# Kernel tuning notes

Hardware: AMD Instinct MI355X
Metric: run time of the kernel (lower is better)

Reference implementation:

```python
import jax, jax.numpy as jnp
import numpy as np

SQRT2 = 1.4142135623730951
T, B, C, H, W = 4, 8, 256, 32, 32
NB, D = 16, 16  # FL_blocks, block_size = dim // FL_blocks
VTH = 0.5       # all l1/l2 spike thresholds default to 0.5
TAUS = (0.01, 0.02, 0.02, 0.05)  # l2 channel-sparsity taus for LL,HL,LH,HH

# Heaviside spike with ATan surrogate gradient (spikingjelly default, alpha=2)
@jax.custom_vjp
def spike(x):
    return (x >= 0.0).astype(x.dtype)

def _spike_fwd(x):
    return spike(x), x

def _spike_bwd(x, g):
    alpha = 2.0
    sg = (alpha / 2.0) / (1.0 + (jnp.pi / 2.0 * alpha * x) ** 2)
    return (g * sg,)

spike.defvjp(_spike_fwd, _spike_bwd)

def lif(x, tau=2.0):
    # MultiStepLIFNode: v += (x - v)/tau, fire at vth=1, hard reset, detach_reset
    def step(v, xt):
        v = v + (xt - v) / tau
        s = spike(v - 1.0)
        v = v * (1.0 - jax.lax.stop_gradient(s))
        return v, s
    _, s = jax.lax.scan(step, jnp.zeros_like(x[0]), x)
    return s

def bn(x, g, b, eps=1e-5):
    # BatchNorm2d in training mode (batch statistics), x: (N,C,H,W)
    m = x.mean((0, 2, 3), keepdims=True)
    v = x.var((0, 2, 3), keepdims=True)
    return (x - m) / jnp.sqrt(v + eps) * g[None, :, None, None] + b[None, :, None, None]

def conv2d(x, w, b):
    y = jax.lax.conv_general_dilated(x, w, (1, 1), 'SAME',
                                     dimension_numbers=('NCHW', 'OIHW', 'NCHW'))
    return y + b[None, :, None, None]

def coeff_gate(c, vth):
    # spike-thresholded wavelet coefficient: keep coeff where |coeff| >= vth
    return c * spike(jnp.abs(c) - vth)

def channel_gate(c, tau):
    # 'channel' sparsity mode: drop whole channels whose mean energy < tau
    e = jnp.mean(c * c, axis=(0, 1, 3, 4))
    return c * spike(e - tau)[None, None, :, None, None]

def fwd(x, haar_weight, conv1_w, conv1_b, conv2_w, conv2_b,
        g_fwd, b_fwd, g_mul, b_mul, g_inv, b_inv, g_c1, b_c1, g_c2, b_c2):
    Tn, Bn, Cn, Hn, Wn = x.shape
    H2, W2 = Hn // 2, Wn // 2
    TB = Tn * Bn
    xs = lif(x)
    # level-1 Haar along W, spike-gated low/high subbands -> (T,B,2C,H,W/2)
    lo = (xs[..., 0::2] + xs[..., 1::2]) / SQRT2
    hi = (xs[..., 0::2] - xs[..., 1::2]) / SQRT2
    h1 = jnp.concatenate([coeff_gate(lo, VTH), coeff_gate(hi, VTH)], axis=2)
    h1 = bn(h1.reshape(TB, 2 * Cn, Hn, W2), g_fwd, b_fwd).reshape(Tn, Bn, 2 * Cn, Hn, W2)
    # level-2 Haar along H -> LL,HL,LH,HH each (T,B,C,H/2,W/2)
    L, Hc = h1[:, :, :Cn], h1[:, :, Cn:]
    def hh(t):
        return ((t[:, :, :, 0::2] + t[:, :, :, 1::2]) / SQRT2,
                (t[:, :, :, 0::2] - t[:, :, :, 1::2]) / SQRT2)
    LL, HL = hh(L)
    LH, HH = hh(Hc)
    subs = [channel_gate(coeff_gate(c, VTH), tau)
            for c, tau in zip((LL, HL, LH, HH), TAUS)]
    h2 = jnp.concatenate(subs, axis=2)  # (T,B,4C,H/2,W/2)
    h2 = bn(h2.reshape(TB, 4 * Cn, H2, W2), g_mul, b_mul).reshape(Tn, Bn, 4 * Cn, H2, W2)
    # block-diagonal mixing: exactly the torch reshape/permute/einsum path
    haar = h2.reshape(TB, NB, 4 * D, H2, W2).transpose(0, 3, 4, 1, 2)  # (TB,H2,W2,NB,4D)
    parts = [jnp.einsum('thwbd,bdk->thwbk', haar[..., i * D:(i + 1) * D], haar_weight)
             for i in range(4)]
    haar = jnp.concatenate(parts, axis=-1)
    haar = haar.reshape(TB, H2, W2, 4 * Cn).transpose(0, 3, 1, 2).reshape(Tn, Bn, 4 * Cn, H2, W2)
    # inverse 2-level Haar -> (T,B,C,H,W)
    LLr, HLr, LHr, HHr = (haar[:, :, i * Cn:(i + 1) * Cn] for i in range(4))
    def inv_h(a, b):
        e = (a + b) / SQRT2
        o = (a - b) / SQRT2
        return jnp.stack([e, o], axis=-2).reshape(Tn, Bn, Cn, Hn, W2)
    Lr = inv_h(LLr, HLr)
    Hr = inv_h(LHr, HHr)
    e = (Lr + Hr) / SQRT2
    o = (Lr - Hr) / SQRT2
    rec = jnp.stack([e, o], axis=-1).reshape(Tn, Bn, Cn, Hn, Wn)
    rec = bn(rec.reshape(TB, Cn, Hn, Wn), g_inv, b_inv).reshape(Tn, Bn, Cn, Hn, Wn)
    # per-block conv residual branches on the spike tensor
    xr = xs.reshape(TB * NB, D, Hn, Wn)
    c1 = bn(conv2d(xr, conv1_w, conv1_b).reshape(TB, Cn, Hn, Wn), g_c1, b_c1).reshape(Tn, Bn, Cn, Hn, Wn)
    c2 = bn(conv2d(xr, conv2_w, conv2_b).reshape(TB, Cn, Hn, Wn), g_c2, b_c2).reshape(Tn, Bn, Cn, Hn, Wn)
    return rec + c1 + c2

def setup_inputs() -> dict:
    key = jax.random.key(0)
    ks = jax.random.split(key, 4)
    return {
        'x': jax.random.normal(ks[0], (T, B, C, H, W), jnp.float32),
        'haar_weight': 0.02 * jax.random.normal(ks[1], (NB, D, D), jnp.float32),
        'conv1_w': 0.1 * jax.random.normal(ks[2], (D, D, 1, 1), jnp.float32),
        'conv1_b': jnp.zeros((D,), jnp.float32),
        'conv2_w': 0.05 * jax.random.normal(ks[3], (D, D, 3, 3), jnp.float32),
        'conv2_b': jnp.zeros((D,), jnp.float32),
        'g_fwd': jnp.ones((2 * C,), jnp.float32), 'b_fwd': jnp.zeros((2 * C,), jnp.float32),
        'g_mul': jnp.ones((4 * C,), jnp.float32), 'b_mul': jnp.zeros((4 * C,), jnp.float32),
        'g_inv': jnp.ones((C,), jnp.float32), 'b_inv': jnp.zeros((C,), jnp.float32),
        'g_c1': jnp.ones((C,), jnp.float32), 'b_c1': jnp.zeros((C,), jnp.float32),
        'g_c2': jnp.ones((C,), jnp.float32), 'b_c2': jnp.zeros((C,), jnp.float32),
    }

def reference(x, haar_weight, conv1_w, conv1_b, conv2_w, conv2_b,
              g_fwd, b_fwd, g_mul, b_mul, g_inv, b_inv, g_c1, b_c1, g_c2, b_c2):
    return fwd(x, haar_weight, conv1_w, conv1_b, conv2_w, conv2_b,
               g_fwd, b_fwd, g_mul, b_mul, g_inv, b_inv, g_c1, b_c1, g_c2, b_c2)
```

## Files before the change

kernel.cpp:

```cpp
#include <hip/hip_runtime.h>

#define T_ 4
#define B_ 8
#define C_ 256
#define TB_ 32
#define SQRT2_ 1.4142135623730951
#define INVS2_ 0.7071067811865475
#define EPS_ 1e-5

typedef __attribute__((ext_vector_type(8))) short short8;
typedef __attribute__((ext_vector_type(4))) float f32x4;

#define XST_OFF  ((size_t)0)
#define H1C_OFF  ((size_t)16777216)
#define COEF_OFF ((size_t)25165824)
#define ST_OFF   ((size_t)41943040)
#define WTAB_OFF ((size_t)42532864)
#define HIST_OFF ((size_t)42555392)
#define S3S 3072
#define S3Q 3328
#define S4S 3584
#define S4Q 3840
#define S5S 4096
#define S5Q 4352
#define NST 4608
#define NREP 16

__device__ __forceinline__ unsigned short f2bf(float v) {
    union { float f; unsigned u; } x; x.f = v;
    unsigned r = x.u + 0x7FFFu + ((x.u >> 16) & 1u);
    return (unsigned short)(r >> 16);
}

__device__ __forceinline__ double st_sum(const double* __restrict__ st, int idx) {
    double s = 0.0;
    #pragma unroll
    for (int r = 0; r < NREP; ++r) s += st[r * NST + idx];
    return s;
}

__device__ __forceinline__ unsigned long long shflx64(unsigned long long v, int m) {
    const unsigned lo_ = __shfl_xor((unsigned)v, m, 64);
    const unsigned hi_ = __shfl_xor((unsigned)(v >> 32), m, 64);
    return ((unsigned long long)hi_ << 32) | lo_;
}

__device__ __forceinline__ void mix_frags_q(const float* __restrict__ hw, int gbq, int lane, short8 am[4]) {
    const int o = lane & 15, g = lane >> 4;
    #pragma unroll
    for (int q = 0; q < 4; ++q) {
        #pragma unroll
        for (int e = 0; e < 8; ++e) {
            const int kk = g * 8 + e;
            unsigned short v = 0;
            if ((kk >> 4) == (q & 1)) {
                const int d = kk & 15;
                const int nbp = q * 4 + gbq;
                v = f2bf(hw[(nbp * 16 + d) * 16 + o]);
            }
            am[q][e] = (short)v;
        }
    }
}

__device__ __forceinline__ void conv_frags(const float* __restrict__ w1, const float* __restrict__ w2w,
                                           int lane, short8* awc2, short8& awc1) {
    const int o = lane & 15, g = lane >> 4, dA = (g & 1) * 8;
    #pragma unroll
    for (int m = 0; m < 5; ++m) {
        const int t = (m < 4) ? (2 * m + (g >> 1)) : 8;
        const bool act = (m < 4) || (g < 2);
        #pragma unroll
        for (int j = 0; j < 8; ++j) {
            const float wv = act ? w2w[(o * 16 + dA + j) * 9 + t] : 0.0f;
            awc2[m][j] = (short)f2bf(wv);
        }
    }
    #pragma unroll
    for (int j = 0; j < 8; ++j) {
        const float wv = (g < 2) ? w1[o * 16 + dA + j] : 0.0f;
        awc1[j] = (short)f2bf(wv);
    }
}

__global__ __launch_bounds__(256) void kwprep(const float* __restrict__ w1, const float* __restrict__ w2w,
                                              const float* __restrict__ hw,
                                              unsigned short* __restrict__ convW,
                                              unsigned short* __restrict__ mixW,
                                              double* __restrict__ st,
                                              int* __restrict__ hist) {
    const int tid = threadIdx.x;
    if (blockIdx.x < 72) {
        const size_t i = ((size_t)blockIdx.x * 256 + tid) * 4;
        double2 z2; z2.x = 0.0; z2.y = 0.0;
        *(double2*)(st + i) = z2;
        *(double2*)(st + i + 2) = z2;
        if (blockIdx.x == 0) {
            const int lane = tid & 63, grp = tid >> 6;
            if (grp == 0) {
                short8 awc2[5], awc1;
                conv_frags(w1, w2w, lane, awc2, awc1);
                #pragma unroll
                for (int m = 0; m < 5; ++m) *(short8*)&convW[(m * 64 + lane) * 8] = awc2[m];
                *(short8*)&convW[(5 * 64 + lane) * 8] = awc1;
            }
            short8 am[4];
            mix_frags_q(hw, grp, lane, am);
            #pragma unroll
            for (int q = 0; q < 4; ++q) *(short8*)&mixW[((grp * 4 + q) * 64 + lane) * 8] = am[q];
        }
    } else {
        const int bi = blockIdx.x - 72;
        uint4* h4 = (uint4*)hist;
        const uint4 z = make_uint4(0u, 0u, 0u, 0u);
        h4[bi * 512 + tid * 2] = z;
        h4[bi * 512 + tid * 2 + 1] = z;
    }
}

__device__ __forceinline__ void load_conv_frags(const unsigned short* __restrict__ convW,
                                                int lane, short8* awc2, short8& awc1) {
    #pragma unroll
    for (int m = 0; m < 5; ++m) awc2[m] = *(const short8*)&convW[(m * 64 + lane) * 8];
    awc1 = *(const short8*)&convW[(5 * 64 + lane) * 8];
}
__device__ __forceinline__ void load_mix_frags(const unsigned short* __restrict__ mixW,
                                               int gbq, int lane, short8 am[4]) {
    #pragma unroll
    for (int q = 0; q < 4; ++q) am[q] = *(const short8*)&mixW[((gbq * 4 + q) * 64 + lane) * 8];
}

__global__ __launch_bounds__(256) void k1_lif(const float* __restrict__ x,
                                              unsigned short* __restrict__ xsT,
                                              signed char* __restrict__ h1c,
                                              int* __restrict__ hist) {
    const int q = blockIdx.x & 3, nb = (blockIdx.x >> 2) & 15, b = blockIdx.x >> 6;
    const int tid = threadIdx.x;
    const int d = tid >> 4, pg = tid & 15;
    const int c = nb * 16 + d;
    const int h = q * 8 + (pg >> 1), wseg = (pg & 1) * 16;
    __shared__ __align__(16) char tr[8192];
    double v[16];
    #pragma unroll
    for (int i = 0; i < 16; ++i) v[i] = 0.0;
    unsigned long long cs = 0, cdd = 0, cu = 0, cv = 0;
    for (int t = 0; t < T_; ++t) {
        const size_t xi = ((size_t)((t * 8 + b) * 256 + c)) * 1024 + h * 32 + wseg;
        const float4* xp = (const float4*)(x + xi);
        int sp[16];
        #pragma unroll
        for (int q4 = 0; q4 < 4; ++q4) {
            const float4 xv = xp[q4];
            #pragma unroll
            for (int e = 0; e < 4; ++e) {
                const double xd = (e == 0 ? xv.x : e == 1 ? xv.y : e == 2 ? xv.z : xv.w);
                double vv = v[q4 * 4 + e];
                vv = vv + (xd - vv) * 0.5;
                const int s = (vv - 1.0 >= 0.0) ? 1 : 0;
                if (s) vv = 0.0;
                v[q4 * 4 + e] = vv;
                sp[q4 * 4 + e] = s;
            }
        }
        unsigned lo8[2] = {0u, 0u}, hi8[2] = {0u, 0u}, hp8[2] = {0u, 0u};
        #pragma unroll
        for (int pr = 0; pr < 8; ++pr) {
            const int lo = sp[2 * pr] + sp[2 * pr + 1];
            const int hi = sp[2 * pr] - sp[2 * pr + 1];
            const int sh = 8 * (pr & 3);
            lo8[pr >> 2] |= (unsigned)(lo & 0xFF) << sh;
            hi8[pr >> 2] |= (unsigned)(hi & 0xFF) << sh;
            hp8[pr >> 2] |= (unsigned)(hi + 1) << sh;
        }
        const size_t lob = ((size_t)((t * 8 + b) * 512 + c)) * 512 + h * 16 + (pg & 1) * 8;
        const size_t hib = ((size_t)((t * 8 + b) * 512 + 256 + c)) * 512 + h * 16 + (pg & 1) * 8;
        *(uint2*)(h1c + lob) = make_uint2(lo8[0], lo8[1]);
        *(uint2*)(h1c + hib) = make_uint2(hi8[0], hi8[1]);
        const unsigned plo0 = __shfl_xor(lo8[0], 2, 64);
        const unsigned plo1 = __shfl_xor(lo8[1], 2, 64);
        const unsigned php0 = __shfl_xor(hp8[0], 2, 64);
        const unsigned php1 = __shfl_xor(hp8[1], 2, 64);
        if (!(pg & 2)) {
            const unsigned sw0 = lo8[0] + plo0, sw1 = lo8[1] + plo1;
            const unsigned dw0 = lo8[0] + (0x02020202u - plo0), dw1 = lo8[1] + (0x02020202u - plo1);
            const unsigned uw0 = hp8[0] + php0, uw1 = hp8[1] + php1;
            const unsigned vw0 = hp8[0] + (0x02020202u - php0), vw1 = hp8[1] + (0x02020202u - php1);
            #pragma unroll
            for (int j = 0; j < 4; ++j) {
                const int sh = 8 * j;
                cs  += 1ull << (12 * ((sw0 >> sh) & 0x7));
                cs  += 1ull << (12 * ((sw1 >> sh) & 0x7));
                cdd += 1ull << (12 * ((dw0 >> sh) & 0x7));
                cdd += 1ull << (12 * ((dw1 >> sh) & 0x7));
                cu  += 1ull << (12 * ((uw0 >> sh) & 0x7));
                cu  += 1ull << (12 * ((uw1 >> sh) & 0x7));
                cv  += 1ull << (12 * ((vw0 >> sh) & 0x7));
                cv  += 1ull << (12 * ((vw1 >> sh) & 0x7));
            }
        }
        unsigned u[8];
        #pragma unroll
        for (int k = 0; k < 8; ++k)
            u[k] = (sp[2 * k] ? 0x3F80u : 0u) | (sp[2 * k + 1] ? 0x3F800000u : 0u);
        const int base = d * 512 + pg * 32;
        const int sw = (d & 3) << 4;
        *(uint4*)(tr + ((base) ^ sw))      = make_uint4(u[0], u[1], u[2], u[3]);
        *(uint4*)(tr + ((base + 16) ^ sw)) = make_uint4(u[4], u[5], u[6], u[7]);
        __syncthreads();
        {
            const int p = tid;
            unsigned o[8];
            #pragma unroll
            for (int dd = 0; dd < 8; ++dd) {
                const unsigned short a0 = *(const unsigned short*)(tr + (2 * dd) * 512 + (((p << 1)) ^ (((2 * dd) & 3) << 4)));
                const unsigned short a1 = *(const unsigned short*)(tr + (2 * dd + 1) * 512 + (((p << 1)) ^ (((2 * dd + 1) & 3) << 4)));
                o[dd] = (unsigned)a0 | ((unsigned)a1 << 16);
            }
            unsigned short* dst = xsT + (((size_t)((t * 8 + b) * 16 + nb)) * 1024 + q * 256 + p) * 16;
            *(uint4*)dst = make_uint4(o[0], o[1], o[2], o[3]);
            *(uint4*)(dst + 8) = make_uint4(o[4], o[5], o[6], o[7]);
        }
        __syncthreads();
    }
    #pragma unroll
    for (int m = 1; m < 16; m <<= 1) {
        cs  += shflx64(cs, m);
        cdd += shflx64(cdd, m);
        cu  += shflx64(cu, m);
        cv  += shflx64(cv, m);
    }
    if (pg == 0) {
        int* hh = hist + ((((b & 3) << 2) | q) * 256 + c) * 20;
        #pragma unroll
        for (int k = 0; k < 5; ++k) {
            atomicAdd(&hh[k],      (int)((cs  >> (12 * k)) & 0xFFF));
            atomicAdd(&hh[5 + k],  (int)((cdd >> (12 * k)) & 0xFFF));
            atomicAdd(&hh[10 + k], (int)((cu  >> (12 * k)) & 0xFFF));
            atomicAdd(&hh[15 + k], (int)((cv  >> (12 * k)) & 0xFFF));
        }
    }
}

__device__ __forceinline__ void conv_tile(const unsigned short* tile, int lane, int h, int w0,
                                          const short8* awc2, const short8& awc1,
                                          f32x4& acc2o, f32x4& acc1o) {
    const int g = lane >> 4, n = lane & 15, dA = (g & 1) * 8;
    short8 bf[6];
    #pragma unroll
    for (int m = 0; m < 6; ++m) {
        const int t = (m < 4) ? (2 * m + (g >> 1)) : ((m == 4) ? 8 : 4);
        const int ky = t / 3, kx = t % 3;
        const int rr = h + ky, cc = w0 + n + kx;
        const int addr = (((rr * 34 + cc) * 32) + dA * 2) ^ ((cc & 4) << 2);
        bf[m] = *(const short8*)((const char*)tile + addr);
    }
    f32x4 acc2 = {0.f, 0.f, 0.f, 0.f};
    #pragma unroll
    for (int m = 0; m < 5; ++m)
        acc2 = __builtin_amdgcn_mfma_f32_16x16x32_bf16(awc2[m], bf[m], acc2, 0, 0, 0);
    const f32x4 z = {0.f, 0.f, 0.f, 0.f};
    acc1o = __builtin_amdgcn_mfma_f32_16x16x32_bf16(awc1, bf[5], z, 0, 0, 0);
    acc2o = acc2;
}

__device__ __forceinline__ void stage_rows(const unsigned short* __restrict__ src,
                                           int r0, int nr, int tid, unsigned short* tile) {
    const int total = nr * 34;
    for (int idx = tid; idx < total; idx += 256) {
        const int r = r0 + idx / 34, cpos = idx % 34;
        const int gh = r - 1, gw = cpos - 1;
        uint4 v0 = make_uint4(0u, 0u, 0u, 0u), v1 = v0;
        if (((unsigned)gh < 32u) & ((unsigned)gw < 32u)) {
            const char* sp = (const char*)(src + (size_t)(gh * 32 + gw) * 16);
            v0 = *(const uint4*)sp;
            v1 = *(const uint4*)(sp + 16);
        }
        const int base = ((r - r0) * 34 + cpos) * 32;
        const int sw = (cpos & 4) << 2;
        *(uint4*)((char*)tile + (base ^ sw)) = v0;
        *(uint4*)((char*)tile + ((base + 16) ^ sw)) = v1;
    }
}

__global__ __launch_bounds__(256) void kmid(const signed char* __restrict__ h1c,
                                            const unsigned short* __restrict__ xsT,
                                            double* __restrict__ st,
                                            char* __restrict__ coefD,
                                            const int* __restrict__ hist,
                                            const unsigned short* __restrict__ mixW,
                                            const unsigned short* __restrict__ convW,
                                            const float* __restrict__ g_fwd, const float* __restrict__ b_fwd,
                                            const float* __restrict__ g_mul, const float* __restrict__ b_mul) {
    __shared__ __align__(16) char smem[15232];
    const int tid = threadIdx.x, lane = tid & 63, wid = tid >> 6;
    if (blockIdx.x < 2048) {
        float* pad = (float*)smem;
        unsigned short* lutL = (unsigned short*)(smem + 512);
        int* histL = (int*)(smem + 1152);
        double* bn1L = (double*)(smem + 2432);
        signed char* rawL = (signed char*)(smem + 2944);
        unsigned short* coefL = (unsigned short*)(smem + 7040);
        const int pb = blockIdx.x & 3, gb = (blockIdx.x >> 2) & 15, tb = blockIdx.x >> 6;
        {
            const int ch = tid >> 3, o8 = (tid & 7) * 16;
            const int cab = (ch < 16) ? gb * 16 + ch : 256 + gb * 16 + (ch - 16);
            *(uint4*)(rawL + ch * 128 + o8) =
                *(const uint4*)(h1c + ((size_t)(tb * 512 + cab)) * 512 + pb * 128 + o8);
        }
        if (tid < 64) {
            const int i = tid & 15, b4 = tid >> 4;
            const int c = gb * 16 + i;
            int cnt[5] = {0, 0, 0, 0, 0};
            for (int rep = 0; rep < NREP; ++rep) {
                const int* hh = hist + (rep * 256 + c) * 20 + b4 * 5;
                #pragma unroll
                for (int k = 0; k < 5; ++k) cnt[k] += hh[k];
            }
            #pragma unroll
            for (int k = 0; k < 5; ++k) histL[i * 20 + b4 * 5 + k] = cnt[k];
        }
        __syncthreads();
        if (tid < 32) {
            const int i = tid & 15, hiF = tid >> 4;
            const int* hl = &histL[i * 20 + hiF * 10];
            double sc = 0.0, s2a = 0.0, s2b = 0.0;
            #pragma unroll
            for (int k = 0; k < 5; ++k) {
                const double c0 = (double)hl[k], c1 = (double)hl[5 + k];
                const int cval = hiF ? (k - 2) : k;
                sc += c0 * cval;
                s2a += c0 * (cval * cval);
                s2b += c1 * ((k - 2) * (k - 2));
            }
            const double sum = sc * INVS2_;
            const double sq = (0.5 * (s2a + s2b)) * 0.5;
            const double m = sum / 16384.0, var = sq / 16384.0 - m * m;
            const int gch = hiF * 256 + gb * 16 + i;
            const double a = (double)g_fwd[gch] / sqrt(var + EPS_);
            bn1L[hiF * 32 + i] = a * INVS2_;
            bn1L[hiF * 32 + 16 + i] = (double)b_fwd[gch] - m * a;
        }
        __syncthreads();
        if (tid < 64) {
            const int i = tid & 15, b4 = tid >> 4;
            const int hiF = b4 >> 1;
            const double A1 = bn1L[hiF * 32 + i], B1 = bn1L[hiF * 32 + 16 + i];
            const int* hl = &histL[i * 20 + b4 * 5];
            double gv[5], S = 0.0, Q = 0.0;
            #pragma unroll
            for (int k = 0; k < 5; ++k) {
                const int code = (b4 == 0) ? k : (k - 2);
                double val = ((b4 & 1) == 0) ? ((double)code * A1 + 2.0 * B1) * INVS2_
                                             : ((double)code * A1) * INVS2_;
                val = (fabs(val) - 0.5 >= 0.0) ? val : 0.0;
                gv[k] = val;
                const double cnt = (double)hl[k];
                S += cnt * val; Q += cnt * val * val;
            }
            const double e = Q / 8192.0;
            const double tau = (b4 == 0) ? 0.01 : (b4 == 3 ? 0.05 : 0.02);
            const int gch = b4 * 256 + gb * 16 + i;
            float A2, B2;
            if (e - tau >= 0.0) {
                const double m = S / 8192.0, var = Q / 8192.0 - m * m;
                const double a = (double)g_mul[gch] / sqrt(var + EPS_);
                A2 = (float)a; B2 = (float)((double)b_mul[gch] - m * a);
            } else { A2 = 0.0f; B2 = b_mul[gch]; }
            #pragma unroll
            for (int k = 0; k < 5; ++k)
                lutL[(i * 4 + b4) * 5 + k] = f2bf(fmaf((float)gv[k], A2, B2));
        }
        __syncthreads();
        {
            const int p = tid & 63, ds = tid >> 6;
            const int h2l = p >> 4, w2 = p & 15;
            unsigned pk[4][2];
            #pragma unroll
            for (int dd = 0; dd < 4; ++dd) {
                const int d = ds * 4 + dd;
                const int base = d * 128 + (2 * h2l) * 16 + w2;
                const int l0 = rawL[base], l1 = rawL[base + 16];
                const int q0 = rawL[2048 + base], q1 = rawL[2048 + base + 16];
                const unsigned short* lp = &lutL[d * 20];
                const unsigned hv[4] = { lp[l0 + l1],
                                         lp[5 + l0 - l1 + 2],
                                         lp[10 + q0 + q1 + 2],
                                         lp[15 + q0 - q1 + 2] };
                #pragma unroll
                for (int q = 0; q < 4; ++q) {
                    if (dd & 1) pk[q][dd >> 1] |= hv[q] << 16;
                    else        pk[q][dd >> 1] = hv[q];
                }
            }
            #pragma unroll
            for (int q = 0; q < 4; ++q) {
                const int slot = (((q & 1) * 2 + (ds >> 1)) ^ (p & 3));
                char* dst = (char*)coefL + (q >> 1) * 4096 + p * 64 + slot * 16 + (ds & 1) * 8;
                *(uint2*)dst = make_uint2(pk[q][0], pk[q][1]);
            }
        }
        short8 am[4];
        load_mix_frags(mixW, gb >> 2, lane, am);
        __syncthreads();
        {
            char* base = coefD + ((size_t)(tb * 16 + gb)) * 32768 + pb * 4096;
            const int i = tid * 32;
            const int pair = i >> 12, loc = i & 4095;
            *(uint4*)(base + pair * 16384 + loc) = *(const uint4*)((const char*)coefL + i);
            *(uint4*)(base + pair * 16384 + loc + 16) = *(const uint4*)((const char*)coefL + i + 16);
        }
        const int o = lane & 15, g = lane >> 4;
        const int Pl = wid * 16 + o;
        f32x4 Mh[4];
        #pragma unroll
        for (int p = 0; p < 2; ++p) {
            const int slot = g ^ (o & 3);
            const short8 bf = *(const short8*)((const char*)coefL + p * 4096 + Pl * 64 + slot * 16);
            const f32x4 z = {0.f, 0.f, 0.f, 0.f};
            Mh[2 * p]     = __builtin_amdgcn_mfma_f32_16x16x32_bf16(am[2 * p], bf, z, 0, 0, 0);
            Mh[2 * p + 1] = __builtin_amdgcn_mfma_f32_16x16x32_bf16(am[2 * p + 1], bf, z, 0, 0, 0);
        }
        float s2x[4], se[4];
        #pragma unroll
        for (int r = 0; r < 4; ++r) {
            s2x[r] = 2.0f * Mh[0][r];
            se[r] = Mh[0][r] * Mh[0][r] + Mh[1][r] * Mh[1][r] + Mh[2][r] * Mh[2][r] + Mh[3][r] * Mh[3][r];
        }
        #pragma unroll
        for (int r = 0; r < 4; ++r)
            #pragma unroll
            for (int m = 1; m < 16; m <<= 1) {
                s2x[r] += __shfl_xor(s2x[r], m, 64);
                se[r]  += __shfl_xor(se[r], m, 64);
            }
        if ((lane & 15) == 0) {
            #pragma unroll
            for (int r = 0; r < 4; ++r) {
                pad[(wid * 16 + g * 4 + r) * 2]     = s2x[r];
                pad[(wid * 16 + g * 4 + r) * 2 + 1] = se[r];
            }
        }
        __syncthreads();
        if (tid < 32) {
            const int j = tid >> 1, s = tid & 1;
            const float tot = pad[(0 * 16 + j) * 2 + s] + pad[(1 * 16 + j) * 2 + s]
                            + pad[(2 * 16 + j) * 2 + s] + pad[(3 * 16 + j) * 2 + s];
            double* stw = st + (((((tb & 3) << 2) | pb)) * NST);
            atomicAdd(&stw[(s ? S3Q : S3S) + gb * 16 + j], (double)tot);
        }
    } else {
        const int bid = blockIdx.x - 2048;
        const int hb = bid & 3, gb = (bid >> 2) & 15, tb = bid >> 6;
        unsigned short* tile = (unsigned short*)smem;
        float* pad = (float*)(smem + 10880);
        const unsigned short* src = xsT + (size_t)(tb * 16 + gb) * 1024 * 16;
        stage_rows(src, hb * 8, 10, tid, tile);
        short8 awc2[5], awc1;
        load_conv_frags(convW, lane, awc2, awc1);
        __syncthreads();
        float t1s[4] = {0, 0, 0, 0}, t1q[4] = {0, 0, 0, 0};
        float t2s[4] = {0, 0, 0, 0}, t2q[4] = {0, 0, 0, 0};
        #pragma unroll
        for (int ti = 0; ti < 4; ++ti) {
            const int lr = wid * 2 + (ti >> 1);
            const int w0 = (ti & 1) * 16;
            f32x4 a2v, a1v;
            conv_tile(tile, lane, lr, w0, awc2, awc1, a2v, a1v);
            #pragma unroll
            for (int r = 0; r < 4; ++r) {
                t1s[r] += a1v[r]; t1q[r] += a1v[r] * a1v[r];
                t2s[r] += a2v[r]; t2q[r] += a2v[r] * a2v[r];
            }
        }
        #pragma unroll
        for (int r = 0; r < 4; ++r)
            #pragma unroll
            for (int m = 1; m < 16; m <<= 1) {
                t1s[r] += __shfl_xor(t1s[r], m, 64);
                t1q[r] += __shfl_xor(t1q[r], m, 64);
                t2s[r] += __shfl_xor(t2s[r], m, 64);
                t2q[r] += __shfl_xor(t2q[r], m, 64);
            }
        if ((lane & 15) == 0) {
            const int G = lane >> 4;
            #pragma unroll
            for (int r = 0; r < 4; ++r) {
                const int oc = G * 4 + r;
                pad[(wid * 16 + oc) * 4 + 0] = t1s[r];
                pad[(wid * 16 + oc) * 4 + 1] = t1q[r];
                pad[(wid * 16 + oc) * 4 + 2] = t2s[r];
                pad[(wid * 16 + oc) * 4 + 3] = t2q[r];
            }
        }
        __syncthreads();
        if (tid < 64) {
            const int oc = tid >> 2, arr = tid & 3;
            const float vv = pad[(0 * 16 + oc) * 4 + arr] + pad[(1 * 16 + oc) * 4 + arr]
                           + pad[(2 * 16 + oc) * 4 + arr] + pad[(3 * 16 + oc) * 4 + arr];
            const int ch = gb * 16 + oc;
            const int off = (arr == 0 ? S4S : arr == 1 ? S4Q : arr == 2 ? S5S : S5Q) + ch;
            double* stw = st + (((((tb & 3) << 2) | hb)) * NST);
            atomicAdd(&stw[off], (double)vv);
        }
    }
}

__global__ __launch_bounds__(256) void kfin(const unsigned short* __restrict__ xsT,
                                            const char* __restrict__ coefD,
                                            const double* __restrict__ st,
                                            const unsigned short* __restrict__ convW,
                                            const unsigned short* __restrict__ mixW,
                                            const float* __restrict__ g_inv, const float* __restrict__ b_inv,
                                            const float* __restrict__ g_c1, const float* __restrict__ b_c1,
                                            const float* __restrict__ g_c2, const float* __restrict__ b_c2,
                                            const float* __restrict__ conv1_b, const float* __restrict__ conv2_b,
                                            float* __restrict__ out) {
    __shared__ __align__(16) char smem[70016];
    const int tid = threadIdx.x, lane = tid & 63, wid = tid >> 6;
    const int tb = blockIdx.x >> 4, gb = blockIdx.x & 15;
    unsigned short* tile  = (unsigned short*)smem;
    unsigned short* coefL = (unsigned short*)(smem + 36992);
    float* PA3 = (float*)(smem + 69760);
    float* PA4 = PA3 + 16; float* PA5 = PA3 + 32; float* PK = PA3 + 48;
    if (tid < 16) {
        const int oc = tid, c = gb * 16 + oc;
        const double n3 = 32768.0;
        const double s3 = st_sum(st, S3S + c), q3 = st_sum(st, S3Q + c);
        const double m3 = s3 / n3, var3 = q3 / n3 - m3 * m3;
        const double a3 = (double)g_inv[c] / sqrt(var3 + EPS_);
        const double bias1 = (double)conv1_b[oc];
        const double s4r = st_sum(st, S4S + c), q4r = st_sum(st, S4Q + c);
        const double s4 = s4r + n3 * bias1;
        const double q4v = q4r + 2.0 * bias1 * s4r + n3 * bias1 * bias1;
        const double m4 = s4 / n3, var4 = q4v / n3 - m4 * m4;
        const double a4 = (double)g_c1[c] / sqrt(var4 + EPS_);
        const double bias2 = (double)conv2_b[oc];
        const double s5r = st_sum(st, S5S + c), q5r = st_sum(st, S5Q + c);
        const double s5 = s5r + n3 * bias2;
        const double q5v = q5r + 2.0 * bias2 * s5r + n3 * bias2 * bias2;
        const double m5 = s5 / n3, var5 = q5v / n3 - m5 * m5;
        const double a5 = (double)g_c2[c] / sqrt(var5 + EPS_);
        PA3[oc] = (float)a3; PA4[oc] = (float)a4; PA5[oc] = (float)a5;
        PK[oc] = (float)(((double)b_inv[c] - m3 * a3) + ((double)b_c1[c] - m4 * a4)
                       + ((double)b_c2[c] - m5 * a5) + a4 * bias1 + a5 * bias2);
    }
    stage_rows(xsT + (size_t)(tb * 16 + gb) * 1024 * 16, 0, 34, tid, tile);
    {
        const char* dump = coefD + ((size_t)(tb * 16 + gb)) * 32768;
        #pragma unroll
        for (int i = 0; i < 8; ++i)
            *(uint4*)((char*)coefL + i * 4096 + tid * 16) = *(const uint4*)(dump + i * 4096 + tid * 16);
    }
    short8 am[4], awc2[5], awc1;
    load_mix_frags(mixW, gb >> 2, lane, am);
    load_conv_frags(convW, lane, awc2, awc1);
    __syncthreads();
    const int G = lane >> 4, n = lane & 15;
    float fA3[4], fA4[4], fA5[4], fK[4];
    #pragma unroll
    for (int r = 0; r < 4; ++r) {
        const int oc = G * 4 + r;
        fA3[r] = PA3[oc]; fA4[r] = PA4[oc]; fA5[r] = PA5[oc]; fK[r] = PK[oc];
    }
    const float sw = (n & 1) ? -1.0f : 1.0f;
    #pragma unroll
    for (int hh = 0; hh < 4; ++hh) {
        f32x4 Mh[4];
        {
            const int o = lane & 15, g = lane >> 4;
            const int P = (wid * 4 + hh) * 16 + o;
            #pragma unroll
            for (int p = 0; p < 2; ++p) {
                const int slot = g ^ (P & 3);
                const short8 bf = *(const short8*)((const char*)coefL + p * 16384 + P * 64 + slot * 16);
                const f32x4 z = {0.f, 0.f, 0.f, 0.f};
                Mh[2 * p]     = __builtin_amdgcn_mfma_f32_16x16x32_bf16(am[2 * p], bf, z, 0, 0, 0);
                Mh[2 * p + 1] = __builtin_amdgcn_mfma_f32_16x16x32_bf16(am[2 * p + 1], bf, z, 0, 0, 0);
            }
        }
        #pragma unroll
        for (int w0h = 0; w0h < 2; ++w0h) {
            const int src = (lane & 48) + w0h * 8 + (n >> 1);
            float ms[4][4];
            #pragma unroll
            for (int q = 0; q < 4; ++q)
                #pragma unroll
                for (int r = 0; r < 4; ++r) ms[q][r] = __shfl(Mh[q][r], src, 64);
            #pragma unroll
            for (int hrow = 0; hrow < 2; ++hrow) {
                const float sh = hrow ? -1.0f : 1.0f;
                const int h = wid * 8 + hh * 2 + hrow;
                const int w0 = w0h * 16;
                f32x4 a2v, a1v;
                conv_tile(tile, lane, h, w0, awc2, awc1, a2v, a1v);
                #pragma unroll
                for (int r = 0; r < 4; ++r) {
                    const float rec = 0.5f * ((ms[0][r] + sh * ms[1][r]) + sw * (ms[2][r] + sh * ms[3][r]));
                    const int oc = G * 4 + r;
                    const size_t ai = ((size_t)(tb * 256 + gb * 16 + oc)) * 1024 + (size_t)h * 32 + w0 + n;
                    out[ai] = fA3[r] * rec + fA4[r] * a1v[r] + fA5[r] * a2v[r] + fK[r];
                }
            }
        }
    }
}

extern "C" void kernel_launch(void* const* d_in, const int* in_sizes, int n_in,
                              void* d_out, int out_size, void* d_ws, size_t ws_size,
                              hipStream_t stream) {
    const float* x        = (const float*)d_in[0];
    const float* haar_w   = (const float*)d_in[1];
    const float* conv1_w  = (const float*)d_in[2];
    const float* conv1_b  = (const float*)d_in[3];
    const float* conv2_w  = (const float*)d_in[4];
    const float* conv2_b  = (const float*)d_in[5];
    const float* g_fwd    = (const float*)d_in[6];
    const float* b_fwd    = (const float*)d_in[7];
    const float* g_mul    = (const float*)d_in[8];
    const float* b_mul    = (const float*)d_in[9];
    const float* g_inv    = (const float*)d_in[10];
    const float* b_inv    = (const float*)d_in[11];
    const float* g_c1     = (const float*)d_in[12];
    const float* b_c1     = (const float*)d_in[13];
    const float* g_c2     = (const float*)d_in[14];
    const float* b_c2     = (const float*)d_in[15];
    float* out = (float*)d_out;

    char* ws = (char*)d_ws;
    unsigned short* xsT = (unsigned short*)(ws + XST_OFF);
    signed char* h1c    = (signed char*)(ws + H1C_OFF);
    char* coefD         = ws + COEF_OFF;
    double* st          = (double*)(ws + ST_OFF);
    unsigned short* convW = (unsigned short*)(ws + WTAB_OFF);
    unsigned short* mixW  = (unsigned short*)(ws + WTAB_OFF + 6144);
    int* hist           = (int*)(ws + HIST_OFF);

    kwprep<<<dim3(112), dim3(256), 0, stream>>>(conv1_w, conv2_w, haar_w, convW, mixW, st, hist);
    k1_lif<<<dim3(512), dim3(256), 0, stream>>>(x, xsT, h1c, hist);
    kmid<<<dim3(4096), dim3(256), 0, stream>>>(h1c, xsT, st, coefD, hist, mixW, convW,
                                               g_fwd, b_fwd, g_mul, b_mul);
    kfin<<<dim3(512), dim3(256), 0, stream>>>(xsT, coefD, st, convW, mixW,
                                              g_inv, b_inv, g_c1, b_c1, g_c2, b_c2,
                                              conv1_b, conv2_b, out);
}
```

Before: 71.07 us.

## Fold prep kernel into LIF kernel, drop histogram atomics, split final kernel by halves

Removes the separate kwprep launch: k1_lif now zeroes the statistics buffer and builds the weight fragment tables itself. The per-channel histogram atomics become plain stores into a 32-replica layout, so the histogram zeroing pass is no longer needed, and kmid sums the replicas instead. kfin is split into two blocks per (tb, group), each handling half the rows, which halves its shared memory use and doubles the grid for better occupancy. In exchange, boundary rows are restaged in each half, and the stats zeroing now relies on kernel ordering within the same launch sequence.

```diff
diff --git a/kernel.cpp b/kernel.cpp
--- a/kernel.cpp
+++ b/kernel.cpp
@@ -25,6 +25,7 @@
 #define S5Q 4352
 #define NST 4608
 #define NREP 16
+#define NHREP 32
 
 __device__ __forceinline__ unsigned short f2bf(float v) {
     union { float f; unsigned u; } x; x.f = v;
@@ -37,12 +38,6 @@
     #pragma unroll
     for (int r = 0; r < NREP; ++r) s += st[r * NST + idx];
     return s;
-}
-
-__device__ __forceinline__ unsigned long long shflx64(unsigned long long v, int m) {
-    const unsigned lo_ = __shfl_xor((unsigned)v, m, 64);
-    const unsigned hi_ = __shfl_xor((unsigned)(v >> 32), m, 64);
-    return ((unsigned long long)hi_ << 32) | lo_;
 }
 
 __device__ __forceinline__ void mix_frags_q(const float* __restrict__ hw, int gbq, int lane, short8 am[4]) {
@@ -83,41 +78,6 @@
     }
 }
 
-__global__ __launch_bounds__(256) void kwprep(const float* __restrict__ w1, const float* __restrict__ w2w,
-                                              const float* __restrict__ hw,
-                                              unsigned short* __restrict__ convW,
-                                              unsigned short* __restrict__ mixW,
-                                              double* __restrict__ st,
-                                              int* __restrict__ hist) {
-    const int tid = threadIdx.x;
-    if (blockIdx.x < 72) {
-        const size_t i = ((size_t)blockIdx.x * 256 + tid) * 4;
-        double2 z2; z2.x = 0.0; z2.y = 0.0;
-        *(double2*)(st + i) = z2;
-        *(double2*)(st + i + 2) = z2;
-        if (blockIdx.x == 0) {
-            const int lane = tid & 63, grp = tid >> 6;
-            if (grp == 0) {
-                short8 awc2[5], awc1;
-                conv_frags(w1, w2w, lane, awc2, awc1);
-                #pragma unroll
-                for (int m = 0; m < 5; ++m) *(short8*)&convW[(m * 64 + lane) * 8] = awc2[m];
-                *(short8*)&convW[(5 * 64 + lane) * 8] = awc1;
-            }
-            short8 am[4];
-            mix_frags_q(hw, grp, lane, am);
-            #pragma unroll
-            for (int q = 0; q < 4; ++q) *(short8*)&mixW[((grp * 4 + q) * 64 + lane) * 8] = am[q];
-        }
-    } else {
-        const int bi = blockIdx.x - 72;
-        uint4* h4 = (uint4*)hist;
-        const uint4 z = make_uint4(0u, 0u, 0u, 0u);
-        h4[bi * 512 + tid * 2] = z;
-        h4[bi * 512 + tid * 2 + 1] = z;
-    }
-}
-
 __device__ __forceinline__ void load_conv_frags(const unsigned short* __restrict__ convW,
                                                 int lane, short8* awc2, short8& awc1) {
     #pragma unroll
@@ -133,9 +93,18 @@
 __global__ __launch_bounds__(256) void k1_lif(const float* __restrict__ x,
                                               unsigned short* __restrict__ xsT,
                                               signed char* __restrict__ h1c,
-                                              int* __restrict__ hist) {
+                                              int* __restrict__ hist,
+                                              double* __restrict__ st,
+                                              const float* __restrict__ w1, const float* __restrict__ w2w,
+                                              const float* __restrict__ hw,
+                                              unsigned short* __restrict__ convW,
+                                              unsigned short* __restrict__ mixW) {
     const int q = blockIdx.x & 3, nb = (blockIdx.x >> 2) & 15, b = blockIdx.x >> 6;
     const int tid = threadIdx.x;
+    if (tid < 72) {
+        double2 z2; z2.x = 0.0; z2.y = 0.0;
+        *(double2*)(st + (size_t)blockIdx.x * 144 + tid * 2) = z2;
+    }
     const int d = tid >> 4, pg = tid & 15;
     const int c = nb * 16 + d;
     const int h = q * 8 + (pg >> 1), wseg = (pg & 1) * 16;
@@ -224,20 +193,50 @@
     }
     #pragma unroll
     for (int m = 1; m < 16; m <<= 1) {
-        cs  += shflx64(cs, m);
-        cdd += shflx64(cdd, m);
-        cu  += shflx64(cu, m);
-        cv  += shflx64(cv, m);
+        {
+            const unsigned a = __shfl_xor((unsigned)cs, m, 64);
+            const unsigned bb2 = __shfl_xor((unsigned)(cs >> 32), m, 64);
+            cs += ((unsigned long long)bb2 << 32) | a;
+        }
+        {
+            const unsigned a = __shfl_xor((unsigned)cdd, m, 64);
+            const unsigned bb2 = __shfl_xor((unsigned)(cdd >> 32), m, 64);
+            cdd += ((unsigned long long)bb2 << 32) | a;
+        }
+        {
+            const unsigned a = __shfl_xor((unsigned)cu, m, 64);
+            const unsigned bb2 = __shfl_xor((unsigned)(cu >> 32), m, 64);
+            cu += ((unsigned long long)bb2 << 32) | a;
+        }
+        {
+            const unsigned a = __shfl_xor((unsigned)cv, m, 64);
+            const unsigned bb2 = __shfl_xor((unsigned)(cv >> 32), m, 64);
+            cv += ((unsigned long long)bb2 << 32) | a;
+        }
     }
     if (pg == 0) {
-        int* hh = hist + ((((b & 3) << 2) | q) * 256 + c) * 20;
+        int* hh = hist + ((size_t)(b * 4 + q) * 20) * 256 + c;
         #pragma unroll
         for (int k = 0; k < 5; ++k) {
-            atomicAdd(&hh[k],      (int)((cs  >> (12 * k)) & 0xFFF));
-            atomicAdd(&hh[5 + k],  (int)((cdd >> (12 * k)) & 0xFFF));
-            atomicAdd(&hh[10 + k], (int)((cu  >> (12 * k)) & 0xFFF));
-            atomicAdd(&hh[15 + k], (int)((cv  >> (12 * k)) & 0xFFF));
-        }
+            hh[k * 256]         = (int)((cs  >> (12 * k)) & 0xFFF);
+            hh[(5 + k) * 256]   = (int)((cdd >> (12 * k)) & 0xFFF);
+            hh[(10 + k) * 256]  = (int)((cu  >> (12 * k)) & 0xFFF);
+            hh[(15 + k) * 256]  = (int)((cv  >> (12 * k)) & 0xFFF);
+        }
+    }
+    if (blockIdx.x == 0) {
+        const int lane = tid & 63, grp = tid >> 6;
+        if (grp == 0) {
+            short8 awc2[5], awc1;
+            conv_frags(w1, w2w, lane, awc2, awc1);
+            #pragma unroll
+            for (int m = 0; m < 5; ++m) *(short8*)&convW[(m * 64 + lane) * 8] = awc2[m];
+            *(short8*)&convW[(5 * 64 + lane) * 8] = awc1;
+        }
+        short8 am[4];
+        mix_frags_q(hw, grp, lane, am);
+        #pragma unroll
+        for (int qq = 0; qq < 4; ++qq) *(short8*)&mixW[((grp * 4 + qq) * 64 + lane) * 8] = am[qq];
     }
 }
 
@@ -307,17 +306,15 @@
             *(uint4*)(rawL + ch * 128 + o8) =
                 *(const uint4*)(h1c + ((size_t)(tb * 512 + cab)) * 512 + pb * 128 + o8);
         }
-        if (tid < 64) {
-            const int i = tid & 15, b4 = tid >> 4;
+        {
+            const int i = tid & 15;
             const int c = gb * 16 + i;
-            int cnt[5] = {0, 0, 0, 0, 0};
-            for (int rep = 0; rep < NREP; ++rep) {
-                const int* hh = hist + (rep * 256 + c) * 20 + b4 * 5;
+            for (int kk = tid >> 4; kk < 20; kk += 16) {
+                int s = 0;
                 #pragma unroll
-                for (int k = 0; k < 5; ++k) cnt[k] += hh[k];
-            }
-            #pragma unroll
-            for (int k = 0; k < 5; ++k) histL[i * 20 + b4 * 5 + k] = cnt[k];
+                for (int rep = 0; rep < NHREP; ++rep) s += hist[((size_t)(rep * 20 + kk)) * 256 + c];
+                histL[i * 20 + kk] = s;
+            }
         }
         __syncthreads();
         if (tid < 32) {
@@ -515,12 +512,12 @@
                                             const float* __restrict__ g_c2, const float* __restrict__ b_c2,
                                             const float* __restrict__ conv1_b, const float* __restrict__ conv2_b,
                                             float* __restrict__ out) {
-    __shared__ __align__(16) char smem[70016];
+    __shared__ __align__(16) char smem[36224];
     const int tid = threadIdx.x, lane = tid & 63, wid = tid >> 6;
-    const int tb = blockIdx.x >> 4, gb = blockIdx.x & 15;
+    const int hf = blockIdx.x & 1, gb = (blockIdx.x >> 1) & 15, tb = blockIdx.x >> 5;
     unsigned short* tile  = (unsigned short*)smem;
-    unsigned short* coefL = (unsigned short*)(smem + 36992);
-    float* PA3 = (float*)(smem + 69760);
+    unsigned short* coefL = (unsigned short*)(smem + 19584);
+    float* PA3 = (float*)(smem + 35968);
     float* PA4 = PA3 + 16; float* PA5 = PA3 + 32; float* PK = PA3 + 48;
     if (tid < 16) {
         const int oc = tid, c = gb * 16 + oc;
@@ -544,12 +541,13 @@
         PK[oc] = (float)(((double)b_inv[c] - m3 * a3) + ((double)b_c1[c] - m4 * a4)
                        + ((double)b_c2[c] - m5 * a5) + a4 * bias1 + a5 * bias2);
     }
-    stage_rows(xsT + (size_t)(tb * 16 + gb) * 1024 * 16, 0, 34, tid, tile);
+    stage_rows(xsT + (size_t)(tb * 16 + gb) * 1024 * 16, hf * 16, 18, tid, tile);
     {
-        const char* dump = coefD + ((size_t)(tb * 16 + gb)) * 32768;
-        #pragma unroll
-        for (int i = 0; i < 8; ++i)
-            *(uint4*)((char*)coefL + i * 4096 + tid * 16) = *(const uint4*)(dump + i * 4096 + tid * 16);
+        const char* dump = coefD + ((size_t)(tb * 16 + gb)) * 32768 + hf * 8192;
+        #pragma unroll
+        for (int i = 0; i < 4; ++i)
+            *(uint4*)((char*)coefL + i * 4096 + tid * 16) =
+                *(const uint4*)(dump + (i >> 1) * 16384 + (i & 1) * 4096 + tid * 16);
     }
     short8 am[4], awc2[5], awc1;
     load_mix_frags(mixW, gb >> 2, lane, am);
@@ -564,15 +562,15 @@
     }
     const float sw = (n & 1) ? -1.0f : 1.0f;
     #pragma unroll
-    for (int hh = 0; hh < 4; ++hh) {
+    for (int hh2 = 0; hh2 < 2; ++hh2) {
         f32x4 Mh[4];
         {
             const int o = lane & 15, g = lane >> 4;
-            const int P = (wid * 4 + hh) * 16 + o;
+            const int Pl = (wid * 2 + hh2) * 16 + o;
             #pragma unroll
             for (int p = 0; p < 2; ++p) {
-                const int slot = g ^ (P & 3);
-                const short8 bf = *(const short8*)((const char*)coefL + p * 16384 + P * 64 + slot * 16);
+                const int slot = g ^ (o & 3);
+                const short8 bf = *(const short8*)((const char*)coefL + p * 8192 + Pl * 64 + slot * 16);
                 const f32x4 z = {0.f, 0.f, 0.f, 0.f};
                 Mh[2 * p]     = __builtin_amdgcn_mfma_f32_16x16x32_bf16(am[2 * p], bf, z, 0, 0, 0);
                 Mh[2 * p + 1] = __builtin_amdgcn_mfma_f32_16x16x32_bf16(am[2 * p + 1], bf, z, 0, 0, 0);
@@ -589,15 +587,16 @@
             #pragma unroll
             for (int hrow = 0; hrow < 2; ++hrow) {
                 const float sh = hrow ? -1.0f : 1.0f;
-                const int h = wid * 8 + hh * 2 + hrow;
+                const int hl = wid * 4 + hh2 * 2 + hrow;
+                const int hglob = hf * 16 + hl;
                 const int w0 = w0h * 16;
                 f32x4 a2v, a1v;
-                conv_tile(tile, lane, h, w0, awc2, awc1, a2v, a1v);
+                conv_tile(tile, lane, hl, w0, awc2, awc1, a2v, a1v);
                 #pragma unroll
                 for (int r = 0; r < 4; ++r) {
                     const float rec = 0.5f * ((ms[0][r] + sh * ms[1][r]) + sw * (ms[2][r] + sh * ms[3][r]));
                     const int oc = G * 4 + r;
-                    const size_t ai = ((size_t)(tb * 256 + gb * 16 + oc)) * 1024 + (size_t)h * 32 + w0 + n;
+                    const size_t ai = ((size_t)(tb * 256 + gb * 16 + oc)) * 1024 + (size_t)hglob * 32 + w0 + n;
                     out[ai] = fA3[r] * rec + fA4[r] * a1v[r] + fA5[r] * a2v[r] + fK[r];
                 }
             }
@@ -635,11 +634,11 @@
     unsigned short* mixW  = (unsigned short*)(ws + WTAB_OFF + 6144);
     int* hist           = (int*)(ws + HIST_OFF);
 
-    kwprep<<<dim3(112), dim3(256), 0, stream>>>(conv1_w, conv2_w, haar_w, convW, mixW, st, hist);
-    k1_lif<<<dim3(512), dim3(256), 0, stream>>>(x, xsT, h1c, hist);
+    k1_lif<<<dim3(512), dim3(256), 0, stream>>>(x, xsT, h1c, hist, st,
+                                                conv1_w, conv2_w, haar_w, convW, mixW);
     kmid<<<dim3(4096), dim3(256), 0, stream>>>(h1c, xsT, st, coefD, hist, mixW, convW,
                                                g_fwd, b_fwd, g_mul, b_mul);
-    kfin<<<dim3(512), dim3(256), 0, stream>>>(xsT, coefD, st, convW, mixW,
-                                              g_inv, b_inv, g_c1, b_c1, g_c2, b_c2,
-                                              conv1_b, conv2_b, out);
-}
+    kfin<<<dim3(1024), dim3(256), 0, stream>>>(xsT, coefD, st, convW, mixW,
+                                               g_inv, b_inv, g_c1, b_c1, g_c2, b_c2,
+                                               conv1_b, conv2_b, out);
+}
```

New measurement: 65.93 us. 1.08x faster.
